# Kernel tuning notes

Measured on AMD Instinct MI355X. Metric: run time of the kernel, lower is better.

## Reference

```python
import jax, jax.numpy as jnp
import numpy as np

B, T, IN, H = 64, 4096, 64, 512
K = 0.5  # 1 / os_factor, os_factor = 2.0


def setup_inputs() -> dict:
    key = jax.random.key(0)
    ks = jax.random.split(key, 5)
    s = 1.0 / np.sqrt(H)  # torch RNNCellBase init scale
    return {
        "x": jax.random.normal(ks[0], (B, T, IN), dtype=jnp.float32),
        "W_ih": jax.random.uniform(ks[1], (4 * H, IN), jnp.float32, -s, s),
        "W_hh": jax.random.uniform(ks[2], (4 * H, H), jnp.float32, -s, s),
        "b_ih": jax.random.uniform(ks[3], (4 * H,), jnp.float32, -s, s),
        "b_hh": jax.random.uniform(ks[4], (4 * H,), jnp.float32, -s, s),
    }


def reference(x, W_ih, W_hh, b_ih, b_hh):
    # STN Euler update around an LSTMCell: s <- s + k*(cell(x, s) - s),
    # where s = [h, c] (state vector). Returns (h states over time, final [h,c]).
    hdim = W_hh.shape[1]
    b = b_ih + b_hh

    def step(carry, xi):
        h, c = carry
        gates = xi @ W_ih.T + h @ W_hh.T + b  # [B, 4H], torch gate order i,f,g,o
        i, f, g, o = jnp.split(gates, 4, axis=-1)
        i = jax.nn.sigmoid(i)
        f = jax.nn.sigmoid(f)
        g = jnp.tanh(g)
        o = jax.nn.sigmoid(o)
        c_new = f * c + i * g
        h_new = o * jnp.tanh(c_new)
        h2 = h + K * (h_new - h)
        c2 = c + K * (c_new - c)
        return (h2, c2), h2

    bsz = x.shape[0]
    h0 = jnp.zeros((bsz, hdim), x.dtype)
    c0 = jnp.zeros((bsz, hdim), x.dtype)
    (hT, cT), hs = jax.lax.scan(step, (h0, c0), jnp.swapaxes(x, 0, 1))
    states = jnp.swapaxes(hs, 0, 1)  # [B, T, H]
    final = jnp.concatenate([hT, cT], axis=-1)  # [B, 2H]
    return states, final
```

## Files before the change

### kernel.cpp

```cpp
#include <hip/hip_runtime.h>


#define Bsz  64
#define Tlen 4096
#define INs  64
#define Hs   512
#define NG   4
#define GB   16
#define RR   32
#define NCH  72

typedef float  floatx4 __attribute__((ext_vector_type(4)));
typedef short  short8  __attribute__((ext_vector_type(8)));

__device__ __forceinline__ unsigned short f2bf(float x) {
    unsigned u = __float_as_uint(x);
    u += 0x7fffu + ((u >> 16) & 1u);
    return (unsigned short)(u >> 16);
}
__device__ __forceinline__ float sigmoidf_(float x) {
    return 1.0f / (1.0f + __expf(-x));
}
__device__ __forceinline__ float tanhf_(float x) {
    return 2.0f / (1.0f + __expf(-2.0f * x)) - 1.0f;
}
__device__ __forceinline__ int hx_idx(int b, int c) { return (b * NCH + (c ^ (b & 7))) * 8; }
__device__ __forceinline__ int w_idx (int r, int c) { return (r * NCH + (c ^ (r & 7))) * 8; }

__global__ __launch_bounds__(256, 2)
void stn_lstm_kernel(const float* __restrict__ x,
                     const float* __restrict__ W_ih,
                     const float* __restrict__ W_hh,
                     const float* __restrict__ b_ih,
                     const float* __restrict__ b_hh,
                     float* __restrict__ out,
                     unsigned* __restrict__ cnt,
                     unsigned* __restrict__ hbuf)
{
    __shared__ unsigned short Wlds[RR * NCH * 8];
    __shared__ unsigned short hx[GB * NCH * 8];
    __shared__ float gates_p[2][RR][17];
    __shared__ float biasL[RR];
    __shared__ unsigned short hpub[GB][8];

    const int tid = threadIdx.x;
    const int bid = blockIdx.x;
    const int g   = bid & 3;
    const int u   = bid >> 2;
    const int bg0 = g * GB;

    for (int idx = tid; idx < RR * Hs / 4; idx += 256) {
        int r  = idx >> 7;
        int k4 = (idx & 127) * 4;
        int Rg = ((r >> 3) << 9) + u * 8 + (r & 7);
        const float4 v = *(const float4*)(W_hh + (size_t)Rg * Hs + k4);
        unsigned short* d = &Wlds[w_idx(r, k4 >> 3) + (k4 & 7)];
        d[0] = f2bf(v.x); d[1] = f2bf(v.y); d[2] = f2bf(v.z); d[3] = f2bf(v.w);
    }
    for (int idx = tid; idx < RR * INs / 4; idx += 256) {
        int r  = idx >> 4;
        int k4 = (idx & 15) * 4;
        int Rg = ((r >> 3) << 9) + u * 8 + (r & 7);
        const float4 v = *(const float4*)(W_ih + (size_t)Rg * INs + k4);
        unsigned short* d = &Wlds[w_idx(r, 64 + (k4 >> 3)) + (k4 & 7)];
        d[0] = f2bf(v.x); d[1] = f2bf(v.y); d[2] = f2bf(v.z); d[3] = f2bf(v.w);
    }
    if (tid < RR) {
        int Rg = ((tid >> 3) << 9) + u * 8 + (tid & 7);
        biasL[tid] = b_ih[Rg] + b_hh[Rg];
    }

    float c_state = 0.0f, h_state = 0.0f;
    const int eb = tid >> 3;
    const int ej = tid & 7;

    const int lane = tid & 63;
    const int wv   = tid >> 6;
    const int nt   = wv >> 1;
    const int kh   = wv & 1;
    const int quad = lane >> 4;
    const int m16  = lane & 15;
    const int rr   = nt * 16 + m16;

    __syncthreads();

    for (int t = 0; t < Tlen; ++t) {
        float4 xv0, xv1;
        if (tid < 128) {
            const float* xp = x + ((size_t)(bg0 + eb) * Tlen + t) * INs + ej * 8;
            xv0 = *(const float4*)xp;
            xv1 = *(const float4*)(xp + 4);
        }

        if (t == 0) {
            int b = tid >> 4, part = tid & 15;
            #pragma unroll
            for (int q = 0; q < 8; ++q)
                ((unsigned long long*)hx)[b * 144 + part * 8 + q] = 0ull;
        } else {
            if (tid == 0) {
                const unsigned tgt = (unsigned)t << 6;
                while (__hip_atomic_load(&cnt[g * 64], __ATOMIC_RELAXED,
                                         __HIP_MEMORY_SCOPE_AGENT) < tgt)
                    __builtin_amdgcn_s_sleep(1);
            }
            __syncthreads();
            const unsigned long long* src = (const unsigned long long*)hbuf
                + ((size_t)(t & 1) * NG + g) * (64 * 32);
            const int b = tid & 15, u0 = tid >> 4;
            unsigned long long v[8];
            #pragma unroll
            for (int r = 0; r < 4; ++r) {
                int uu = u0 + 16 * r;
                v[2 * r]     = __hip_atomic_load(src + uu * 32 + b * 2,
                                   __ATOMIC_RELAXED, __HIP_MEMORY_SCOPE_SYSTEM);
                v[2 * r + 1] = __hip_atomic_load(src + uu * 32 + b * 2 + 1,
                                   __ATOMIC_RELAXED, __HIP_MEMORY_SCOPE_SYSTEM);
            }
            #pragma unroll
            for (int r = 0; r < 4; ++r) {
                int uu = u0 + 16 * r;
                *(unsigned long long*)&hx[hx_idx(b, uu)]     = v[2 * r];
                *(unsigned long long*)&hx[hx_idx(b, uu) + 4] = v[2 * r + 1];
            }
        }
        if (tid < 128) {
            unsigned short* d = &hx[hx_idx(eb, 64 + ej)];
            d[0] = f2bf(xv0.x); d[1] = f2bf(xv0.y); d[2] = f2bf(xv0.z); d[3] = f2bf(xv0.w);
            d[4] = f2bf(xv1.x); d[5] = f2bf(xv1.y); d[6] = f2bf(xv1.z); d[7] = f2bf(xv1.w);
        }
        __syncthreads();

        {
            floatx4 acc = {0.f, 0.f, 0.f, 0.f};
            #pragma unroll
            for (int kt = 0; kt < 9; ++kt) {
                int c = (kh * 9 + kt) * 4 + quad;
                short8 af = *(const short8*)&hx[hx_idx(m16, c)];
                short8 bf = *(const short8*)&Wlds[w_idx(rr, c)];
                acc = __builtin_amdgcn_mfma_f32_16x16x32_bf16(af, bf, acc, 0, 0, 0);
            }
            #pragma unroll
            for (int r2 = 0; r2 < 4; ++r2)
                gates_p[kh][rr][quad * 4 + r2] = acc[r2];
        }
        __syncthreads();

        if (tid < 128) {
            float gi = gates_p[0][ej][eb]      + gates_p[1][ej][eb]      + biasL[ej];
            float gf = gates_p[0][8 + ej][eb]  + gates_p[1][8 + ej][eb]  + biasL[8 + ej];
            float gg = gates_p[0][16 + ej][eb] + gates_p[1][16 + ej][eb] + biasL[16 + ej];
            float go = gates_p[0][24 + ej][eb] + gates_p[1][24 + ej][eb] + biasL[24 + ej];
            float ii = sigmoidf_(gi);
            float ff = sigmoidf_(gf);
            float gv = tanhf_(gg);
            float oo = sigmoidf_(go);
            float c_new = ff * c_state + ii * gv;
            float h_new = oo * tanhf_(c_new);
            float h2 = 0.5f * (h_state + h_new);
            float c2 = 0.5f * (c_state + c_new);
            h_state = h2; c_state = c2;
            __builtin_nontemporal_store(h2,
                &out[((size_t)(bg0 + eb) * Tlen + t) * Hs + (u * 8 + ej)]);
            hpub[eb][ej] = f2bf(h2);
        }
        __syncthreads();

        if (tid < 64) {
            int b = tid >> 2, jp = tid & 3;
            unsigned w32 = (unsigned)hpub[b][jp * 2] | ((unsigned)hpub[b][jp * 2 + 1] << 16);
            size_t o = (((size_t)((t + 1) & 1) * NG + g) * 64 + (size_t)u) * 64 + b * 4 + jp;
            __hip_atomic_store(&hbuf[o], w32, __ATOMIC_RELAXED, __HIP_MEMORY_SCOPE_SYSTEM);
        }
        __builtin_amdgcn_s_waitcnt(0x0f70);
        __syncthreads();
        if (tid == 0)
            __hip_atomic_fetch_add(&cnt[g * 64], 1u,
                                   __ATOMIC_RELAXED, __HIP_MEMORY_SCOPE_AGENT);
    }

    if (tid < 128) {
        size_t base = (size_t)Bsz * Tlen * Hs;
        int bgl = bg0 + eb;
        out[base + (size_t)bgl * 1024 + (u * 8 + ej)]       = h_state;
        out[base + (size_t)bgl * 1024 + 512 + (u * 8 + ej)] = c_state;
    }
}

extern "C" void kernel_launch(void* const* d_in, const int* in_sizes, int n_in,
                              void* d_out, int out_size, void* d_ws, size_t ws_size,
                              hipStream_t stream) {
    (void)in_sizes; (void)n_in; (void)out_size; (void)ws_size;
    const float* x    = (const float*)d_in[0];
    const float* W_ih = (const float*)d_in[1];
    const float* W_hh = (const float*)d_in[2];
    const float* b_ih = (const float*)d_in[3];
    const float* b_hh = (const float*)d_in[4];
    float* out = (float*)d_out;
    unsigned* cnt  = (unsigned*)d_ws;
    unsigned* hbuf = (unsigned*)((char*)d_ws + 1024);
    hipMemsetAsync(d_ws, 0, 1024, stream);
    hipLaunchKernelGGL(stn_lstm_kernel, dim3(256), dim3(256), 0, stream,
                       x, W_ih, W_hh, b_ih, b_hh, out, cnt, hbuf);
}
```

Baseline: 11.79 ms.

## Hold weights in registers, load h directly into MFMA operands, per-block flags

Keeps each wave's bf16 weight fragments in registers and loads the previous hidden state from the global exchange buffer straight into MFMA A operands, skipping the LDS staging of h and W. It replaces the shared atomic counter with per-block flags that each wave polls, and drops several block-wide barriers per step by double-buffering the gate scratch. The input projection is folded in as extra MFMA k-tiles, and bias goes into the accumulator. The aim is a shorter serial critical path per timestep, at the cost of more register pressure (occupancy 1) and heavier polling traffic.

```diff
diff --git a/kernel.cpp b/kernel.cpp
--- a/kernel.cpp
+++ b/kernel.cpp
@@ -8,10 +8,11 @@
 #define NG   4
 #define GB   16
 #define RR   32
-#define NCH  72
 
 typedef float  floatx4 __attribute__((ext_vector_type(4)));
+typedef float  floatx2 __attribute__((ext_vector_type(2)));
 typedef short  short8  __attribute__((ext_vector_type(8)));
+typedef unsigned long long u64;
 
 __device__ __forceinline__ unsigned short f2bf(float x) {
     unsigned u = __float_as_uint(x);
@@ -24,55 +25,24 @@
 __device__ __forceinline__ float tanhf_(float x) {
     return 2.0f / (1.0f + __expf(-2.0f * x)) - 1.0f;
 }
-__device__ __forceinline__ int hx_idx(int b, int c) { return (b * NCH + (c ^ (b & 7))) * 8; }
-__device__ __forceinline__ int w_idx (int r, int c) { return (r * NCH + (c ^ (r & 7))) * 8; }
-
-__global__ __launch_bounds__(256, 2)
+
+__global__ __launch_bounds__(256, 1)
 void stn_lstm_kernel(const float* __restrict__ x,
                      const float* __restrict__ W_ih,
                      const float* __restrict__ W_hh,
                      const float* __restrict__ b_ih,
                      const float* __restrict__ b_hh,
                      float* __restrict__ out,
-                     unsigned* __restrict__ cnt,
-                     unsigned* __restrict__ hbuf)
+                     unsigned* __restrict__ flags,
+                     u64* __restrict__ hbuf)
 {
-    __shared__ unsigned short Wlds[RR * NCH * 8];
-    __shared__ unsigned short hx[GB * NCH * 8];
-    __shared__ float gates_p[2][RR][17];
-    __shared__ float biasL[RR];
-    __shared__ unsigned short hpub[GB][8];
+    __shared__ float gates_p[2][2][RR][17];
 
     const int tid = threadIdx.x;
     const int bid = blockIdx.x;
     const int g   = bid & 3;
     const int u   = bid >> 2;
     const int bg0 = g * GB;
-
-    for (int idx = tid; idx < RR * Hs / 4; idx += 256) {
-        int r  = idx >> 7;
-        int k4 = (idx & 127) * 4;
-        int Rg = ((r >> 3) << 9) + u * 8 + (r & 7);
-        const float4 v = *(const float4*)(W_hh + (size_t)Rg * Hs + k4);
-        unsigned short* d = &Wlds[w_idx(r, k4 >> 3) + (k4 & 7)];
-        d[0] = f2bf(v.x); d[1] = f2bf(v.y); d[2] = f2bf(v.z); d[3] = f2bf(v.w);
-    }
-    for (int idx = tid; idx < RR * INs / 4; idx += 256) {
-        int r  = idx >> 4;
-        int k4 = (idx & 15) * 4;
-        int Rg = ((r >> 3) << 9) + u * 8 + (r & 7);
-        const float4 v = *(const float4*)(W_ih + (size_t)Rg * INs + k4);
-        unsigned short* d = &Wlds[w_idx(r, 64 + (k4 >> 3)) + (k4 & 7)];
-        d[0] = f2bf(v.x); d[1] = f2bf(v.y); d[2] = f2bf(v.z); d[3] = f2bf(v.w);
-    }
-    if (tid < RR) {
-        int Rg = ((tid >> 3) << 9) + u * 8 + (tid & 7);
-        biasL[tid] = b_ih[Rg] + b_hh[Rg];
-    }
-
-    float c_state = 0.0f, h_state = 0.0f;
-    const int eb = tid >> 3;
-    const int ej = tid & 7;
 
     const int lane = tid & 63;
     const int wv   = tid >> 6;
@@ -82,108 +52,134 @@
     const int m16  = lane & 15;
     const int rr   = nt * 16 + m16;
 
-    __syncthreads();
+    const int Rg = ((rr >> 3) << 9) + u * 8 + (rr & 7);
+    short8 wreg[9];
+    #pragma unroll
+    for (int kt = 0; kt < 9; ++kt) {
+        const int c = kh * 36 + kt * 4 + quad;
+        const float* src = (c < 64) ? (W_hh + (size_t)Rg * Hs + c * 8)
+                                    : (W_ih + (size_t)Rg * INs + (c - 64) * 8);
+        short8 w;
+        #pragma unroll
+        for (int e = 0; e < 8; ++e) w[e] = (short)f2bf(src[e]);
+        wreg[kt] = w;
+    }
+    const float bv = (kh == 0) ? (b_ih[Rg] + b_hh[Rg]) : 0.0f;
+
+    const float* xp = x + (size_t)(bg0 + m16) * Tlen * INs;
+
+    const int eb = tid >> 2;
+    const int jp = tid & 3;
+    float h0s = 0.f, c0s = 0.f, h1s = 0.f, c1s = 0.f;
+    float* op = out + (size_t)(bg0 + eb) * Tlen * Hs + u * 8 + 2 * jp;
+
+    const bool pollmask = (kh == 0) ? (lane < 36) : (lane >= 36);
 
     for (int t = 0; t < Tlen; ++t) {
-        float4 xv0, xv1;
-        if (tid < 128) {
-            const float* xp = x + ((size_t)(bg0 + eb) * Tlen + t) * INs + ej * 8;
-            xv0 = *(const float4*)xp;
-            xv1 = *(const float4*)(xp + 4);
-        }
-
-        if (t == 0) {
-            int b = tid >> 4, part = tid & 15;
-            #pragma unroll
-            for (int q = 0; q < 8; ++q)
-                ((unsigned long long*)hx)[b * 144 + part * 8 + q] = 0ull;
-        } else {
-            if (tid == 0) {
-                const unsigned tgt = (unsigned)t << 6;
-                while (__hip_atomic_load(&cnt[g * 64], __ATOMIC_RELAXED,
-                                         __HIP_MEMORY_SCOPE_AGENT) < tgt)
-                    __builtin_amdgcn_s_sleep(1);
-            }
-            __syncthreads();
-            const unsigned long long* src = (const unsigned long long*)hbuf
-                + ((size_t)(t & 1) * NG + g) * (64 * 32);
-            const int b = tid & 15, u0 = tid >> 4;
-            unsigned long long v[8];
-            #pragma unroll
-            for (int r = 0; r < 4; ++r) {
-                int uu = u0 + 16 * r;
-                v[2 * r]     = __hip_atomic_load(src + uu * 32 + b * 2,
-                                   __ATOMIC_RELAXED, __HIP_MEMORY_SCOPE_SYSTEM);
-                v[2 * r + 1] = __hip_atomic_load(src + uu * 32 + b * 2 + 1,
-                                   __ATOMIC_RELAXED, __HIP_MEMORY_SCOPE_SYSTEM);
-            }
-            #pragma unroll
-            for (int r = 0; r < 4; ++r) {
-                int uu = u0 + 16 * r;
-                *(unsigned long long*)&hx[hx_idx(b, uu)]     = v[2 * r];
-                *(unsigned long long*)&hx[hx_idx(b, uu) + 4] = v[2 * r + 1];
-            }
-        }
-        if (tid < 128) {
-            unsigned short* d = &hx[hx_idx(eb, 64 + ej)];
-            d[0] = f2bf(xv0.x); d[1] = f2bf(xv0.y); d[2] = f2bf(xv0.z); d[3] = f2bf(xv0.w);
-            d[4] = f2bf(xv1.x); d[5] = f2bf(xv1.y); d[6] = f2bf(xv1.z); d[7] = f2bf(xv1.w);
-        }
-        __syncthreads();
-
+        const int par = t & 1;
+
+        floatx4 xa, xb, xc, xd;
+        if (kh == 1) {
+            xa = *(const floatx4*)(xp + quad * 8);
+            xb = *(const floatx4*)(xp + quad * 8 + 4);
+            xc = *(const floatx4*)(xp + 32 + quad * 8);
+            xd = *(const floatx4*)(xp + 32 + quad * 8 + 4);
+            xp += INs;
+        }
+
+        if (t > 0) {
+            const unsigned tgt = (unsigned)t;
+            unsigned f;
+            do {
+                f = __hip_atomic_load(&flags[g * 64 + lane], __ATOMIC_RELAXED,
+                                      __HIP_MEMORY_SCOPE_AGENT);
+            } while (__any(pollmask && (f < tgt)));
+        }
+        __builtin_amdgcn_sched_barrier(0);
+
+        u64 p0[9], p1[9];
         {
-            floatx4 acc = {0.f, 0.f, 0.f, 0.f};
+            const size_t rb = ((size_t)par * NG + g) * 64;
             #pragma unroll
             for (int kt = 0; kt < 9; ++kt) {
-                int c = (kh * 9 + kt) * 4 + quad;
-                short8 af = *(const short8*)&hx[hx_idx(m16, c)];
-                short8 bf = *(const short8*)&Wlds[w_idx(rr, c)];
-                acc = __builtin_amdgcn_mfma_f32_16x16x32_bf16(af, bf, acc, 0, 0, 0);
+                if (kt < 7 || kh == 0) {
+                    const int c = kh * 36 + kt * 4 + quad;
+                    const u64* q = hbuf + (rb + c) * 32 + m16 * 2;
+                    p0[kt] = __hip_atomic_load(q,     __ATOMIC_RELAXED, __HIP_MEMORY_SCOPE_SYSTEM);
+                    p1[kt] = __hip_atomic_load(q + 1, __ATOMIC_RELAXED, __HIP_MEMORY_SCOPE_SYSTEM);
+                }
             }
-            #pragma unroll
-            for (int r2 = 0; r2 < 4; ++r2)
-                gates_p[kh][rr][quad * 4 + r2] = acc[r2];
-        }
+        }
+
+        floatx4 acc0 = {bv, bv, bv, bv};
+        floatx4 acc1 = {0.f, 0.f, 0.f, 0.f};
+        #pragma unroll
+        for (int kt = 0; kt < 9; ++kt) {
+            short8 af;
+            if (kt >= 7 && kh == 1) {
+                const floatx4 lo = (kt == 7) ? xa : xc;
+                const floatx4 hi = (kt == 7) ? xb : xd;
+                af[0] = (short)f2bf(lo[0]); af[1] = (short)f2bf(lo[1]);
+                af[2] = (short)f2bf(lo[2]); af[3] = (short)f2bf(lo[3]);
+                af[4] = (short)f2bf(hi[0]); af[5] = (short)f2bf(hi[1]);
+                af[6] = (short)f2bf(hi[2]); af[7] = (short)f2bf(hi[3]);
+            } else {
+                union { u64 q[2]; short8 s; } cv;
+                cv.q[0] = p0[kt]; cv.q[1] = p1[kt];
+                af = cv.s;
+            }
+            if (kt & 1) acc1 = __builtin_amdgcn_mfma_f32_16x16x32_bf16(af, wreg[kt], acc1, 0, 0, 0);
+            else        acc0 = __builtin_amdgcn_mfma_f32_16x16x32_bf16(af, wreg[kt], acc0, 0, 0, 0);
+        }
+        const floatx4 acc = acc0 + acc1;
+        #pragma unroll
+        for (int r2 = 0; r2 < 4; ++r2)
+            gates_p[par][kh][rr][quad * 4 + r2] = acc[r2];
+
         __syncthreads();
 
-        if (tid < 128) {
-            float gi = gates_p[0][ej][eb]      + gates_p[1][ej][eb]      + biasL[ej];
-            float gf = gates_p[0][8 + ej][eb]  + gates_p[1][8 + ej][eb]  + biasL[8 + ej];
-            float gg = gates_p[0][16 + ej][eb] + gates_p[1][16 + ej][eb] + biasL[16 + ej];
-            float go = gates_p[0][24 + ej][eb] + gates_p[1][24 + ej][eb] + biasL[24 + ej];
-            float ii = sigmoidf_(gi);
-            float ff = sigmoidf_(gf);
-            float gv = tanhf_(gg);
-            float oo = sigmoidf_(go);
-            float c_new = ff * c_state + ii * gv;
-            float h_new = oo * tanhf_(c_new);
-            float h2 = 0.5f * (h_state + h_new);
-            float c2 = 0.5f * (c_state + c_new);
-            h_state = h2; c_state = c2;
-            __builtin_nontemporal_store(h2,
-                &out[((size_t)(bg0 + eb) * Tlen + t) * Hs + (u * 8 + ej)]);
-            hpub[eb][ej] = f2bf(h2);
-        }
-        __syncthreads();
-
         if (tid < 64) {
-            int b = tid >> 2, jp = tid & 3;
-            unsigned w32 = (unsigned)hpub[b][jp * 2] | ((unsigned)hpub[b][jp * 2 + 1] << 16);
-            size_t o = (((size_t)((t + 1) & 1) * NG + g) * 64 + (size_t)u) * 64 + b * 4 + jp;
-            __hip_atomic_store(&hbuf[o], w32, __ATOMIC_RELAXED, __HIP_MEMORY_SCOPE_SYSTEM);
-        }
-        __builtin_amdgcn_s_waitcnt(0x0f70);
-        __syncthreads();
-        if (tid == 0)
-            __hip_atomic_fetch_add(&cnt[g * 64], 1u,
+            const int e0 = 2 * jp, e1 = e0 + 1;
+            const float gi0 = gates_p[par][0][e0][eb]      + gates_p[par][1][e0][eb];
+            const float gf0 = gates_p[par][0][8 + e0][eb]  + gates_p[par][1][8 + e0][eb];
+            const float gg0 = gates_p[par][0][16 + e0][eb] + gates_p[par][1][16 + e0][eb];
+            const float go0 = gates_p[par][0][24 + e0][eb] + gates_p[par][1][24 + e0][eb];
+            const float gi1 = gates_p[par][0][e1][eb]      + gates_p[par][1][e1][eb];
+            const float gf1 = gates_p[par][0][8 + e1][eb]  + gates_p[par][1][8 + e1][eb];
+            const float gg1 = gates_p[par][0][16 + e1][eb] + gates_p[par][1][16 + e1][eb];
+            const float go1 = gates_p[par][0][24 + e1][eb] + gates_p[par][1][24 + e1][eb];
+
+            const float cn0 = sigmoidf_(gf0) * c0s + sigmoidf_(gi0) * tanhf_(gg0);
+            const float hn0 = sigmoidf_(go0) * tanhf_(cn0);
+            const float cn1 = sigmoidf_(gf1) * c1s + sigmoidf_(gi1) * tanhf_(gg1);
+            const float hn1 = sigmoidf_(go1) * tanhf_(cn1);
+            const float h20 = 0.5f * (h0s + hn0), c20 = 0.5f * (c0s + cn0);
+            const float h21 = 0.5f * (h1s + hn1), c21 = 0.5f * (c1s + cn1);
+            h0s = h20; c0s = c20; h1s = h21; c1s = c21;
+
+            const unsigned w = (unsigned)f2bf(h20) | ((unsigned)f2bf(h21) << 16);
+            const size_t widx = (((size_t)(par ^ 1) * NG + g) * 64 + u) * 64 + eb * 4 + jp;
+            __hip_atomic_store((unsigned*)hbuf + widx, w, __ATOMIC_RELAXED,
+                               __HIP_MEMORY_SCOPE_SYSTEM);
+            __builtin_amdgcn_sched_barrier(0);
+            __builtin_amdgcn_s_waitcnt(0x0f70);
+            __builtin_amdgcn_sched_barrier(0);
+            if (tid == 0)
+                __hip_atomic_store(&flags[g * 64 + u], (unsigned)(t + 1),
                                    __ATOMIC_RELAXED, __HIP_MEMORY_SCOPE_AGENT);
+            floatx2 ov; ov[0] = h20; ov[1] = h21;
+            __builtin_nontemporal_store(ov, (floatx2*)op);
+            op += Hs;
+        }
     }
 
-    if (tid < 128) {
-        size_t base = (size_t)Bsz * Tlen * Hs;
-        int bgl = bg0 + eb;
-        out[base + (size_t)bgl * 1024 + (u * 8 + ej)]       = h_state;
-        out[base + (size_t)bgl * 1024 + 512 + (u * 8 + ej)] = c_state;
+    if (tid < 64) {
+        const size_t base = (size_t)Bsz * Tlen * Hs;
+        float* fp = out + base + (size_t)(bg0 + eb) * 1024 + u * 8 + 2 * jp;
+        floatx2 hv; hv[0] = h0s; hv[1] = h1s;
+        floatx2 cv; cv[0] = c0s; cv[1] = c1s;
+        *(floatx2*)fp = hv;
+        *(floatx2*)(fp + 512) = cv;
     }
 }
 
@@ -197,9 +193,9 @@
     const float* b_ih = (const float*)d_in[3];
     const float* b_hh = (const float*)d_in[4];
     float* out = (float*)d_out;
-    unsigned* cnt  = (unsigned*)d_ws;
-    unsigned* hbuf = (unsigned*)((char*)d_ws + 1024);
-    hipMemsetAsync(d_ws, 0, 1024, stream);
+    unsigned* flags = (unsigned*)d_ws;
+    u64* hbuf = (u64*)((char*)d_ws + 1024);
+    hipMemsetAsync(d_ws, 0, 1024 + 65536, stream);
     hipLaunchKernelGGL(stn_lstm_kernel, dim3(256), dim3(256), 0, stream,
-                       x, W_ih, W_hh, b_ih, b_hh, out, cnt, hbuf);
-}
+                       x, W_ih, W_hh, b_ih, b_hh, out, flags, hbuf);
+}
```

Result: slower. 22.02 ms (+86.8%).
